# Kernel optimization log

Hardware: AMD Instinct MI355X
Metric: run time of the kernel (lower is better)

Reference implementation:

```python
import jax, jax.numpy as jnp
import numpy as np

B, N, C = 2, 2048, 1024
H = 16
DH = C // H
LN_EPS = 1e-5
NEG = -1e20


def setup_inputs() -> dict:
    key = jax.random.key(0)
    ks = jax.random.split(key, 8)
    s = 1.0 / np.sqrt(C)
    return {
        "query": jax.random.normal(ks[0], (B, N, C), dtype=jnp.float32),
        "key": jax.random.normal(ks[1], (B, N, C), dtype=jnp.float32),
        "value": jax.random.normal(ks[2], (B, N, C), dtype=jnp.float32),
        "attn_mask": jnp.ones((B, N), dtype=bool),
        # torch nn.Linear weights are [out, in]; y = x @ W.T
        "Wq": jax.random.uniform(ks[3], (C, C), jnp.float32, -s, s),
        "Wk": jax.random.uniform(ks[4], (C, C), jnp.float32, -s, s),
        "Wv": jax.random.uniform(ks[5], (C, C), jnp.float32, -s, s),
        "Wo": jax.random.uniform(ks[6], (C, C), jnp.float32, -s, s),
        "ln_g": jnp.ones((C,), jnp.float32),
        "ln_b": jnp.zeros((C,), jnp.float32),
    }


def reference(query, key, value, attn_mask, Wq, Wk, Wv, Wo, ln_g, ln_b):
    residual = query
    # projections + head split: [B,N,C] -> [B,H,N,DH]
    q = (query @ Wq.T).reshape(B, N, H, DH).transpose(0, 2, 1, 3)
    k = (key @ Wk.T).reshape(B, N, H, DH).transpose(0, 2, 1, 3)
    v = (value @ Wv.T).reshape(B, N, H, DH).transpose(0, 2, 1, 3)
    # NOTE: source computes scale but never applies it
    scores = jnp.einsum("bhqd,bhkd->bhqk", q, k)  # [B,H,N,N]
    # self-attention branch: outer-product mask [B,N,N]
    m2 = attn_mask[:, :, None] & attn_mask[:, None, :]
    scores = jnp.where(m2[:, None, :, :], scores, NEG)
    # NOTE: source uses nn.Softmax(dim=2) on 4D tensor -> softmax over QUERY axis
    attn = jax.nn.softmax(scores, axis=2)
    ctx = jnp.einsum("bhqk,bhkd->bhqd", attn, v)  # [B,H,N,DH]
    ctx = ctx.transpose(0, 2, 1, 3).reshape(B, N, C)
    out = ctx @ Wo.T
    x = residual + out
    mu = jnp.mean(x, axis=-1, keepdims=True)
    var = jnp.var(x, axis=-1, keepdims=True)
    return (x - mu) * jax.lax.rsqrt(var + LN_EPS) * ln_g + ln_b
```

## Files before the change

kernel.cpp:

```cpp
#include <hip/hip_runtime.h>
#include <hip/hip_bf16.h>

#define Bb 2
#define Nn 2048
#define Cc 1024
#define Hh 16
#define DHh 64

#define LOG2E 1.44269504088896340736f

typedef __attribute__((ext_vector_type(8))) short s16x8;
typedef __attribute__((ext_vector_type(4))) float f32x4;
typedef __attribute__((ext_vector_type(16))) float f32x16;

__device__ inline unsigned short f2bf(float f) {
  union { float f; unsigned u; } v; v.f = f;
  unsigned r = v.u + 0x7FFFu + ((v.u >> 16) & 1u);
  return (unsigned short)(r >> 16);
}
__device__ inline float bf2f(unsigned short h) {
  union { unsigned u; float f; } v; v.u = ((unsigned)h) << 16;
  return v.f;
}
__device__ inline float fast_exp2(float x) { return __builtin_amdgcn_exp2f(x); }

__device__ inline void gload16(const unsigned short* g, unsigned short* lds) {
  __builtin_amdgcn_global_load_lds(
      (const __attribute__((address_space(1))) unsigned int*)g,
      (__attribute__((address_space(3))) unsigned int*)lds, 16, 0, 0);
}

__device__ inline void barrier_lds_only() {
  asm volatile("s_waitcnt lgkmcnt(0)" ::: "memory");
  __builtin_amdgcn_s_barrier();
}

__device__ inline f32x4 mfma16(s16x8 a, s16x8 b, f32x4 c) {
  return __builtin_amdgcn_mfma_f32_16x16x32_bf16(a, b, c, 0, 0, 0);
}
__device__ inline f32x16 mfma32(s16x8 a, s16x8 b, f32x16 c) {
  return __builtin_amdgcn_mfma_f32_32x32x16_bf16(a, b, c, 0, 0, 0);
}

struct ConvArgs {
  const float* src[7];
  unsigned short* dst[7];
  int n[7];
  float scale[7];
};
__global__ __launch_bounds__(256) void conv_bf16(ConvArgs a) {
  const int y = blockIdx.y;
  const float* __restrict__ s = a.src[y];
  unsigned short* __restrict__ d = a.dst[y];
  const int n4 = a.n[y] >> 2;
  const float sc = a.scale[y];
  for (int i = blockIdx.x * 256 + threadIdx.x; i < n4; i += 1024 * 256) {
    f32x4 v = *(const f32x4*)(s + 4 * (size_t)i);
    ushort4 o;
    o.x = f2bf(v.x * sc); o.y = f2bf(v.y * sc);
    o.z = f2bf(v.z * sc); o.w = f2bf(v.w * sc);
    *(ushort4*)(d + 4 * (size_t)i) = o;
  }
}

__global__ __launch_bounds__(256) void gemm_qkv_bb(
    const unsigned short* __restrict__ Aq, const unsigned short* __restrict__ Ak,
    const unsigned short* __restrict__ Av,
    const unsigned short* __restrict__ Bq, const unsigned short* __restrict__ Bk,
    const unsigned short* __restrict__ Bv,
    unsigned short* __restrict__ Yq, unsigned short* __restrict__ Yk,
    unsigned short* __restrict__ Yv)
{
  __shared__ unsigned short As[3][128][32];
  __shared__ unsigned short Bs[3][128][32];

  const int bid = blockIdx.x + 8 * (blockIdx.y + 32 * blockIdx.z);
  const int swz = (bid & 7) * 96 + (bid >> 3);
  const int bx = swz & 7, by = (swz >> 3) & 31, bz = swz >> 8;

  const unsigned short* A = (bz == 0) ? Aq : (bz == 1) ? Ak : Av;
  const unsigned short* Bw = (bz == 0) ? Bq : (bz == 1) ? Bk : Bv;
  unsigned short* Y = (bz == 0) ? Yq : (bz == 1) ? Yk : Yv;

  const int tid = threadIdx.x;
  const int lane = tid & 63, wid = tid >> 6;
  const int r = lane & 15, g = lane >> 4;
  const int wr = wid >> 1, wc = wid & 1;
  const int m_blk = by * 128, n_blk = bx * 128;

  const int gr = wid * 16 + (lane >> 2);
  const int gc = (lane & 3) * 8;

  f32x4 acc[4][4] = {};

#pragma unroll
  for (int p = 0; p < 3; ++p) {
    gload16(A  + (size_t)(m_blk + gr)      * Cc + p * 32 + gc, &As[p][wid * 16][0]);
    gload16(A  + (size_t)(m_blk + 64 + gr) * Cc + p * 32 + gc, &As[p][64 + wid * 16][0]);
    gload16(Bw + (size_t)(n_blk + gr)      * Cc + p * 32 + gc, &Bs[p][wid * 16][0]);
    gload16(Bw + (size_t)(n_blk + 64 + gr) * Cc + p * 32 + gc, &Bs[p][64 + wid * 16][0]);
  }

  int cur = 0;
  for (int kt = 0; kt < 32; ++kt) {
    asm volatile("s_waitcnt vmcnt(8)" ::: "memory");
    __builtin_amdgcn_s_barrier();
    s16x8 av[4], bv[4];
#pragma unroll
    for (int i = 0; i < 4; ++i) av[i] = *(const s16x8*)&As[cur][wr * 64 + 16 * i + r][g * 8];
#pragma unroll
    for (int j = 0; j < 4; ++j) bv[j] = *(const s16x8*)&Bs[cur][wc * 64 + 16 * j + r][g * 8];
#pragma unroll
    for (int i = 0; i < 4; ++i)
#pragma unroll
      for (int j = 0; j < 4; ++j) acc[i][j] = mfma16(av[i], bv[j], acc[i][j]);
    asm volatile("s_barrier" ::: "memory");
    const int kn = (kt + 3 < 32) ? (kt + 3) * 32 : 0;
    gload16(A  + (size_t)(m_blk + gr)      * Cc + kn + gc, &As[cur][wid * 16][0]);
    gload16(A  + (size_t)(m_blk + 64 + gr) * Cc + kn + gc, &As[cur][64 + wid * 16][0]);
    gload16(Bw + (size_t)(n_blk + gr)      * Cc + kn + gc, &Bs[cur][wid * 16][0]);
    gload16(Bw + (size_t)(n_blk + 64 + gr) * Cc + kn + gc, &Bs[cur][64 + wid * 16][0]);
    cur = (cur == 2) ? 0 : cur + 1;
  }
#pragma unroll
  for (int i = 0; i < 4; ++i)
#pragma unroll
    for (int j = 0; j < 4; ++j)
#pragma unroll
      for (int t = 0; t < 4; ++t) {
        int row = m_blk + wr * 64 + 16 * i + 4 * g + t;
        int col = n_blk + wc * 64 + 16 * j + r;
        Y[(size_t)row * Cc + col] = f2bf(acc[i][j][t]);
      }
}

__global__ __launch_bounds__(256) void col_exp_fused(
    const unsigned short* __restrict__ Qb, const unsigned short* __restrict__ Kb,
    const unsigned short* __restrict__ Vb, unsigned short* __restrict__ Vtg)
{
  __shared__ unsigned short Qc[2][128][72];
  __shared__ float lsum[128];
  __shared__ float rl[128];
  const int tid = threadIdx.x;
  const int lane = tid & 63, w = tid >> 6;
  const int r = lane & 15, g = lane >> 4;
  const int k0 = blockIdx.x * 128;
  const int h = blockIdx.y, b = blockIdx.z;
  const size_t base = (size_t)b * Nn * Cc + (size_t)h * DHh;

  if (tid < 128) lsum[tid] = 0.f;
  s16x8 bv[2][8];
#pragma unroll
  for (int s = 0; s < 2; ++s)
#pragma unroll
    for (int j = 0; j < 8; ++j)
      bv[s][j] = *(const s16x8*)(Kb + base + (size_t)(k0 + 16 * j + r) * Cc + s * 32 + g * 8);

  const int srow = tid >> 3, sc8 = (tid & 7) * 8;
  s16x8 rQ[4];
#pragma unroll
  for (int it = 0; it < 4; ++it)
    rQ[it] = *(const s16x8*)(Qb + base + (size_t)(srow + 32 * it) * Cc + sc8);
#pragma unroll
  for (int it = 0; it < 4; ++it)
    *(s16x8*)&Qc[0][srow + 32 * it][sc8] = rQ[it];
#pragma unroll
  for (int it = 0; it < 4; ++it)
    rQ[it] = *(const s16x8*)(Qb + base + (size_t)(128 + srow + 32 * it) * Cc + sc8);
  __syncthreads();

  float esum[8] = {};
  for (int qc = 0; qc < Nn / 128; ++qc) {
    const int cur = qc & 1, nxt = cur ^ 1;
#pragma unroll
    for (int it = 0; it < 4; ++it)
      *(s16x8*)&Qc[nxt][srow + 32 * it][sc8] = rQ[it];
    s16x8 av[2][2];
#pragma unroll
    for (int s = 0; s < 2; ++s)
#pragma unroll
      for (int i = 0; i < 2; ++i)
        av[s][i] = *(const s16x8*)&Qc[cur][w * 32 + 16 * i + r][s * 32 + g * 8];
    const int qn = (qc + 2 < Nn / 128) ? (qc + 2) * 128 : 0;
#pragma unroll
    for (int it = 0; it < 4; ++it)
      rQ[it] = *(const s16x8*)(Qb + base + (size_t)(qn + srow + 32 * it) * Cc + sc8);
    f32x4 acc[2][8] = {};
    __builtin_amdgcn_s_setprio(1);
#pragma unroll
    for (int s = 0; s < 2; ++s)
#pragma unroll
      for (int i = 0; i < 2; ++i)
#pragma unroll
        for (int j = 0; j < 4; ++j) acc[i][j] = mfma16(av[s][i], bv[s][j], acc[i][j]);
    __builtin_amdgcn_s_setprio(0);
#pragma unroll
    for (int j = 0; j < 4; ++j)
#pragma unroll
      for (int i = 0; i < 2; ++i)
#pragma unroll
        for (int t = 0; t < 4; ++t) esum[j] += fast_exp2(acc[i][j][t]);
    __builtin_amdgcn_s_setprio(1);
#pragma unroll
    for (int s = 0; s < 2; ++s)
#pragma unroll
      for (int i = 0; i < 2; ++i)
#pragma unroll
        for (int j = 4; j < 8; ++j) acc[i][j] = mfma16(av[s][i], bv[s][j], acc[i][j]);
    __builtin_amdgcn_s_setprio(0);
#pragma unroll
    for (int j = 4; j < 8; ++j)
#pragma unroll
      for (int i = 0; i < 2; ++i)
#pragma unroll
        for (int t = 0; t < 4; ++t) esum[j] += fast_exp2(acc[i][j][t]);
    barrier_lds_only();
  }
#pragma unroll
  for (int j = 0; j < 8; ++j) {
    float e = esum[j];
    e += __shfl_xor(e, 16, 64);
    e += __shfl_xor(e, 32, 64);
    if (g == 0) atomicAdd(&lsum[16 * j + r], e);
  }
  __syncthreads();
  if (tid < 128) rl[tid] = 1.0f / lsum[tid];
  __syncthreads();
#pragma unroll
  for (int it = 0; it < 4; ++it) {
    int e = tid + 256 * it;
    int row = e >> 3, c8 = (e & 7) * 8;
    *(s16x8*)&Qc[0][row][c8] = *(const s16x8*)(Vb + base + (size_t)(k0 + row) * Cc + c8);
  }
  __syncthreads();
  const size_t vbase = (size_t)(b * Hh + h) * DHh * Nn;
#pragma unroll
  for (int it = 0; it < 4; ++it) {
    int f = tid + 256 * it;
    int d = f >> 4;
    int p8 = (f & 15) * 8;
    int sg = p8 >> 4;
    int hl = (p8 >> 3) & 1;
    s16x8 o;
#pragma unroll
    for (int u = 0; u < 8; ++u) {
      int k = 16 * sg + 4 * hl + (u & 3) + 8 * (u >> 2);
      o[u] = (short)f2bf(bf2f(Qc[0][k][d]) * rl[k]);
    }
    *(s16x8*)(Vtg + vbase + (size_t)d * Nn + k0 + p8) = o;
  }
}

__global__ __launch_bounds__(256, 4) void ctx_pv(
    const unsigned short* __restrict__ Qb, const unsigned short* __restrict__ Kb,
    const unsigned short* __restrict__ Vtg,
    unsigned short* __restrict__ Ctx0, unsigned short* __restrict__ Ctx1)
{
  __shared__ unsigned short Kt[2][64][72];
  __shared__ unsigned short Vt[2][64][72];
  const int tid = threadIdx.x;
  const int lane = tid & 63, w = tid >> 6;
  const int m = lane & 31;
  const int hl = lane >> 5;
  const int q0 = blockIdx.x * 128;
  const int h = blockIdx.y;
  const int b = blockIdx.z >> 1, half = blockIdx.z & 1;
  const int kstart = half * (Nn / 2);
  const size_t base = (size_t)b * Nn * Cc + (size_t)h * DHh;
  const size_t vbase = (size_t)(b * Hh + h) * DHh * Nn;

  s16x8 av[4];
#pragma unroll
  for (int s = 0; s < 4; ++s)
    av[s] = *(const s16x8*)(Qb + base + (size_t)(q0 + w * 32 + m) * Cc + s * 16 + hl * 8);

  const int srow = tid >> 3, sc8 = (tid & 7) * 8;
  s16x8 rK[2], rV[2];
#pragma unroll
  for (int it = 0; it < 2; ++it) {
    rK[it] = *(const s16x8*)(Kb + base + (size_t)(kstart + srow + 32 * it) * Cc + sc8);
    rV[it] = *(const s16x8*)(Vtg + vbase + (size_t)(srow + 32 * it) * Nn + kstart + sc8);
  }
#pragma unroll
  for (int it = 0; it < 2; ++it) {
    *(s16x8*)&Kt[0][srow + 32 * it][sc8] = rK[it];
    *(s16x8*)&Vt[0][srow + 32 * it][sc8] = rV[it];
  }
#pragma unroll
  for (int it = 0; it < 2; ++it) {
    rK[it] = *(const s16x8*)(Kb + base + (size_t)(kstart + 64 + srow + 32 * it) * Cc + sc8);
    rV[it] = *(const s16x8*)(Vtg + vbase + (size_t)(srow + 32 * it) * Nn + kstart + 64 + sc8);
  }
  __syncthreads();

  f32x16 acc2[2] = {};

  for (int kt = 0; kt < 16; ++kt) {
    const int cur = kt & 1, nxt = cur ^ 1;
#pragma unroll
    for (int it = 0; it < 2; ++it) {
      *(s16x8*)&Kt[nxt][srow + 32 * it][sc8] = rK[it];
      *(s16x8*)&Vt[nxt][srow + 32 * it][sc8] = rV[it];
    }
    const int kn = kstart + ((kt + 2 < 16) ? (kt + 2) * 64 : 0);
#pragma unroll
    for (int it = 0; it < 2; ++it) {
      rK[it] = *(const s16x8*)(Kb + base + (size_t)(kn + srow + 32 * it) * Cc + sc8);
      rV[it] = *(const s16x8*)(Vtg + vbase + (size_t)(srow + 32 * it) * Nn + kn + sc8);
    }
    f32x16 sa0 = {};
    __builtin_amdgcn_s_setprio(1);
#pragma unroll
    for (int s = 0; s < 4; ++s) {
      s16x8 kv = *(const s16x8*)&Kt[cur][m][s * 16 + hl * 8];
      sa0 = mfma32(kv, av[s], sa0);
    }
    __builtin_amdgcn_s_setprio(0);
    f32x16 sa1 = {};
    __builtin_amdgcn_s_setprio(1);
#pragma unroll
    for (int s = 0; s < 4; ++s) {
      s16x8 kv = *(const s16x8*)&Kt[cur][32 + m][s * 16 + hl * 8];
      sa1 = mfma32(kv, av[s], sa1);
    }
    __builtin_amdgcn_s_setprio(0);
    union { s16x8 v; unsigned int u[4]; } pf0[2];
#pragma unroll
    for (int g2 = 0; g2 < 2; ++g2)
#pragma unroll
      for (int p = 0; p < 4; ++p) {
        float e0 = fast_exp2(sa0[8 * g2 + 2 * p]);
        float e1 = fast_exp2(sa0[8 * g2 + 2 * p + 1]);
        pf0[g2].u[p] = __builtin_amdgcn_perm(__float_as_uint(e1), __float_as_uint(e0),
                                             0x07060302u);
      }
    __builtin_amdgcn_s_setprio(1);
#pragma unroll
    for (int g2 = 0; g2 < 2; ++g2)
#pragma unroll
      for (int j2 = 0; j2 < 2; ++j2) {
        s16x8 bv = *(const s16x8*)&Vt[cur][32 * j2 + m][g2 * 16 + hl * 8];
        acc2[j2] = mfma32(pf0[g2].v, bv, acc2[j2]);
      }
    __builtin_amdgcn_s_setprio(0);
    union { s16x8 v; unsigned int u[4]; } pf1[2];
#pragma unroll
    for (int g2 = 0; g2 < 2; ++g2)
#pragma unroll
      for (int p = 0; p < 4; ++p) {
        float e0 = fast_exp2(sa1[8 * g2 + 2 * p]);
        float e1 = fast_exp2(sa1[8 * g2 + 2 * p + 1]);
        pf1[g2].u[p] = __builtin_amdgcn_perm(__float_as_uint(e1), __float_as_uint(e0),
                                             0x07060302u);
      }
    __builtin_amdgcn_s_setprio(1);
#pragma unroll
    for (int g2 = 0; g2 < 2; ++g2)
#pragma unroll
      for (int j2 = 0; j2 < 2; ++j2) {
        s16x8 bv = *(const s16x8*)&Vt[cur][32 * j2 + m][(2 + g2) * 16 + hl * 8];
        acc2[j2] = mfma32(pf1[g2].v, bv, acc2[j2]);
      }
    __builtin_amdgcn_s_setprio(0);
    barrier_lds_only();
  }
  unsigned short* __restrict__ Cg = half ? Ctx1 : Ctx0;
#pragma unroll
  for (int j2 = 0; j2 < 2; ++j2)
#pragma unroll
    for (int t = 0; t < 16; ++t) {
      int qr = 32 * w + (t & 3) + 8 * (t >> 2) + 4 * hl;
      Cg[base + (size_t)(q0 + qr) * Cc + 32 * j2 + m] = f2bf(acc2[j2][t]);
    }
}

__global__ __launch_bounds__(512) void gemm_res_bb(
    const unsigned short* __restrict__ A0, const unsigned short* __restrict__ A1,
    const unsigned short* __restrict__ Bw,
    const float* __restrict__ resid, float* __restrict__ Yout)
{
  __shared__ unsigned short As[2][128][32];
  __shared__ unsigned short Bs[2][64][32];

  const int bid0 = blockIdx.x + 16 * blockIdx.y;
  const int swz = (bid0 & 7) * 64 + (bid0 >> 3);
  const int bx = swz & 15, by = swz >> 4;
  const int m_blk = by * 128, n_blk = bx * 64;

  const int tid = threadIdx.x;
  const int lane = tid & 63, wid = tid >> 6;
  const int r = lane & 15, g = lane >> 4;
  const int wr = wid >> 1, wc = wid & 1;

  const int arow = tid >> 2, ac8 = (tid & 3) * 8;
  const int grb = (wid & 3) * 16 + (lane >> 2), gcb = (lane & 3) * 8;

  f32x4 acc[2][2] = {};

  s16x8 rA0 = *(const s16x8*)(A0 + (size_t)(m_blk + arow) * Cc + ac8);
  s16x8 rA1 = *(const s16x8*)(A1 + (size_t)(m_blk + arow) * Cc + ac8);
  if (wid < 4)
    gload16(Bw + (size_t)(n_blk + grb) * Cc + gcb, &Bs[0][(wid & 3) * 16][0]);
  {
    s16x8 s0;
#pragma unroll
    for (int u = 0; u < 8; ++u)
      s0[u] = (short)f2bf(bf2f((unsigned short)rA0[u]) + bf2f((unsigned short)rA1[u]));
    *(s16x8*)&As[0][arow][ac8] = s0;
  }
  rA0 = *(const s16x8*)(A0 + (size_t)(m_blk + arow) * Cc + 32 + ac8);
  rA1 = *(const s16x8*)(A1 + (size_t)(m_blk + arow) * Cc + 32 + ac8);
  __syncthreads();

  int cur = 0;
  for (int k0 = 0; k0 < Cc; k0 += 32) {
    const int nxt = cur ^ 1;
    const int kn  = (k0 + 32 < Cc) ? k0 + 32 : 0;
    const int kn2 = (k0 + 64 < Cc) ? k0 + 64 : 0;
    if (wid < 4)
      gload16(Bw + (size_t)(n_blk + grb) * Cc + kn + gcb, &Bs[nxt][(wid & 3) * 16][0]);
    s16x8 nA0 = *(const s16x8*)(A0 + (size_t)(m_blk + arow) * Cc + kn2 + ac8);
    s16x8 nA1 = *(const s16x8*)(A1 + (size_t)(m_blk + arow) * Cc + kn2 + ac8);
    {
      s16x8 s0;
#pragma unroll
      for (int u = 0; u < 8; ++u)
        s0[u] = (short)f2bf(bf2f((unsigned short)rA0[u]) + bf2f((unsigned short)rA1[u]));
      *(s16x8*)&As[nxt][arow][ac8] = s0;
    }
    s16x8 av[2], bvv[2];
#pragma unroll
    for (int i = 0; i < 2; ++i) av[i] = *(const s16x8*)&As[cur][wr * 32 + 16 * i + r][g * 8];
#pragma unroll
    for (int j = 0; j < 2; ++j) bvv[j] = *(const s16x8*)&Bs[cur][wc * 32 + 16 * j + r][g * 8];
#pragma unroll
    for (int i = 0; i < 2; ++i)
#pragma unroll
      for (int j = 0; j < 2; ++j) acc[i][j] = mfma16(av[i], bvv[j], acc[i][j]);
    rA0 = nA0; rA1 = nA1;
    __syncthreads();
    cur = nxt;
  }
#pragma unroll
  for (int i = 0; i < 2; ++i)
#pragma unroll
    for (int j = 0; j < 2; ++j)
#pragma unroll
      for (int t = 0; t < 4; ++t) {
        size_t idx = (size_t)(m_blk + wr * 32 + 16 * i + 4 * g + t) * Cc
                   + (n_blk + wc * 32 + 16 * j + r);
        Yout[idx] = acc[i][j][t] + resid[idx];
      }
}

__global__ __launch_bounds__(256) void layernorm_inplace(
    float* __restrict__ X, const float* __restrict__ gam, const float* __restrict__ bet)
{
  const int row = blockIdx.x;
  const int tid = threadIdx.x;
  float* x = X + (size_t)row * Cc;
  f32x4 v = *(const f32x4*)(x + tid * 4);
  float s = v.x + v.y + v.z + v.w;
  float ss = v.x * v.x + v.y * v.y + v.z * v.z + v.w * v.w;
#pragma unroll
  for (int m = 1; m < 64; m <<= 1) { s += __shfl_xor(s, m, 64); ss += __shfl_xor(ss, m, 64); }
  __shared__ float red[8];
  const int w = tid >> 6, lane = tid & 63;
  if (lane == 0) { red[w] = s; red[4 + w] = ss; }
  __syncthreads();
  s  = red[0] + red[1] + red[2] + red[3];
  ss = red[4] + red[5] + red[6] + red[7];
  const float mean = s * (1.f / Cc);
  const float var  = ss * (1.f / Cc) - mean * mean;
  const float inv  = rsqrtf(var + 1e-5f);
  f32x4 gv = *(const f32x4*)(gam + tid * 4);
  f32x4 bv = *(const f32x4*)(bet + tid * 4);
  f32x4 o;
  o.x = (v.x - mean) * inv * gv.x + bv.x;
  o.y = (v.y - mean) * inv * gv.y + bv.y;
  o.z = (v.z - mean) * inv * gv.z + bv.z;
  o.w = (v.w - mean) * inv * gv.w + bv.w;
  *(f32x4*)(x + tid * 4) = o;
}

__global__ __launch_bounds__(256) void gemm_qkv_fb(
    const float* __restrict__ Xq, const float* __restrict__ Xk, const float* __restrict__ Xv,
    const float* __restrict__ Wq, const float* __restrict__ Wk, const float* __restrict__ Wv,
    unsigned short* __restrict__ Yq, unsigned short* __restrict__ Yk, unsigned short* __restrict__ Yv)
{
  __shared__ unsigned short As[128][40];
  __shared__ unsigned short Bs[128][40];
  const int z = blockIdx.z;
  const float* X = (z == 0) ? Xq : (z == 1) ? Xk : Xv;
  const float* W = (z == 0) ? Wq : (z == 1) ? Wk : Wv;
  unsigned short* Y = (z == 0) ? Yq : (z == 1) ? Yk : Yv;
  const float scale = (z == 0) ? LOG2E : 1.0f;

  const int tid = threadIdx.x;
  const int lane = tid & 63, wid = tid >> 6;
  const int r = lane & 15, g = lane >> 4;
  const int wr = wid >> 1, wc = wid & 1;
  const int m_blk = blockIdx.y * 128, n_blk = blockIdx.x * 128;

  f32x4 acc[4][4] = {};

  for (int k0 = 0; k0 < Cc; k0 += 32) {
    __syncthreads();
#pragma unroll
    for (int it = 0; it < 4; ++it) {
      int f = tid + 256 * it;
      int row = f >> 3, c4 = (f & 7) * 4;
      f32x4 xa = *(const f32x4*)(X + (size_t)(m_blk + row) * Cc + k0 + c4);
      ushort4 pa; pa.x = f2bf(xa.x); pa.y = f2bf(xa.y); pa.z = f2bf(xa.z); pa.w = f2bf(xa.w);
      *(ushort4*)&As[row][c4] = pa;
      f32x4 xb = *(const f32x4*)(W + (size_t)(n_blk + row) * Cc + k0 + c4);
      ushort4 pb; pb.x = f2bf(xb.x); pb.y = f2bf(xb.y); pb.z = f2bf(xb.z); pb.w = f2bf(xb.w);
      *(ushort4*)&Bs[row][c4] = pb;
    }
    __syncthreads();
    s16x8 av[4], bv[4];
#pragma unroll
    for (int i = 0; i < 4; ++i) av[i] = *(const s16x8*)&As[wr * 64 + 16 * i + r][g * 8];
#pragma unroll
    for (int j = 0; j < 4; ++j) bv[j] = *(const s16x8*)&Bs[wc * 64 + 16 * j + r][g * 8];
#pragma unroll
    for (int i = 0; i < 4; ++i)
#pragma unroll
      for (int j = 0; j < 4; ++j) acc[i][j] = mfma16(av[i], bv[j], acc[i][j]);
  }
#pragma unroll
  for (int i = 0; i < 4; ++i)
#pragma unroll
    for (int j = 0; j < 4; ++j)
#pragma unroll
      for (int t = 0; t < 4; ++t) {
        int row = m_blk + wr * 64 + 16 * i + 4 * g + t;
        int col = n_blk + wc * 64 + 16 * j + r;
        Y[(size_t)row * Cc + col] = f2bf(acc[i][j][t] * scale);
      }
}

__global__ __launch_bounds__(256) void ctx_pv_fb(
    const unsigned short* __restrict__ Qb, const unsigned short* __restrict__ Kb,
    const unsigned short* __restrict__ Vtg, unsigned short* __restrict__ Ctx)
{
  __shared__ unsigned short Kt[64][72];
  __shared__ unsigned short Vt[64][72];
  __shared__ unsigned short Qs[128][72];
  const int tid = threadIdx.x;
  const int lane = tid & 63, w = tid >> 6;
  const int m = lane & 31;
  const int hl = lane >> 5;
  const int q0 = blockIdx.x * 128;
  const int h = blockIdx.y, b = blockIdx.z;
  const size_t base = (size_t)b * Nn * Cc + (size_t)h * DHh;
  const size_t vbase = (size_t)(b * Hh + h) * DHh * Nn;

#pragma unroll
  for (int it = 0; it < 4; ++it) {
    int e = tid + 256 * it;
    int row = e >> 3, c8 = (e & 7) * 8;
    *(s16x8*)&Qs[row][c8] = *(const s16x8*)(Qb + base + (size_t)(q0 + row) * Cc + c8);
  }
  __syncthreads();
  s16x8 av[4];
#pragma unroll
  for (int s = 0; s < 4; ++s) av[s] = *(const s16x8*)&Qs[w * 32 + m][s * 16 + hl * 8];

  const int srow = tid >> 3, sc8 = (tid & 7) * 8;
  s16x8 rK[2], rV[2];
#pragma unroll
  for (int it = 0; it < 2; ++it) {
    rK[it] = *(const s16x8*)(Kb + base + (size_t)(srow + 32 * it) * Cc + sc8);
    rV[it] = *(const s16x8*)(Vtg + vbase + (size_t)(srow + 32 * it) * Nn + sc8);
  }

  f32x16 acc2[2] = {};

  for (int kt = 0; kt < Nn / 64; ++kt) {
    __syncthreads();
#pragma unroll
    for (int it = 0; it < 2; ++it) {
      *(s16x8*)&Kt[srow + 32 * it][sc8] = rK[it];
      *(s16x8*)&Vt[srow + 32 * it][sc8] = rV[it];
    }
    const int kn = (kt + 1 < Nn / 64) ? (kt + 1) * 64 : 0;
#pragma unroll
    for (int it = 0; it < 2; ++it) {
      rK[it] = *(const s16x8*)(Kb + base + (size_t)(kn + srow + 32 * it) * Cc + sc8);
      rV[it] = *(const s16x8*)(Vtg + vbase + (size_t)(srow + 32 * it) * Nn + kn + sc8);
    }
    __syncthreads();
#pragma unroll
    for (int kj = 0; kj < 2; ++kj) {
      f32x16 sa = {};
#pragma unroll
      for (int s = 0; s < 4; ++s) {
        s16x8 kv = *(const s16x8*)&Kt[32 * kj + m][s * 16 + hl * 8];
        sa = mfma32(kv, av[s], sa);
      }
#pragma unroll
      for (int g2 = 0; g2 < 2; ++g2) {
        union { s16x8 v; unsigned int u[4]; } pf;
#pragma unroll
        for (int p = 0; p < 4; ++p) {
          float e0 = fast_exp2(sa[8 * g2 + 2 * p]);
          float e1 = fast_exp2(sa[8 * g2 + 2 * p + 1]);
          pf.u[p] = __builtin_amdgcn_perm(__float_as_uint(e1), __float_as_uint(e0),
                                          0x07060302u);
        }
        const int sg = 2 * kj + g2;
#pragma unroll
        for (int j2 = 0; j2 < 2; ++j2) {
          s16x8 bv = *(const s16x8*)&Vt[32 * j2 + m][sg * 16 + hl * 8];
          acc2[j2] = mfma32(pf.v, bv, acc2[j2]);
        }
      }
    }
  }
#pragma unroll
  for (int j2 = 0; j2 < 2; ++j2)
#pragma unroll
    for (int t = 0; t < 16; ++t) {
      int qr = 32 * w + (t & 3) + 8 * (t >> 2) + 4 * hl;
      Ctx[base + (size_t)(q0 + qr) * Cc + 32 * j2 + m] = f2bf(acc2[j2][t]);
    }
}

__global__ __launch_bounds__(256) void gemm_res_fb(
    const unsigned short* __restrict__ Xb, const float* __restrict__ W,
    const float* __restrict__ resid, float* __restrict__ Yout)
{
  __shared__ unsigned short As[128][40];
  __shared__ unsigned short Bs[128][40];
  const int tid = threadIdx.x;
  const int lane = tid & 63, wid = tid >> 6;
  const int r = lane & 15, g = lane >> 4;
  const int wr = wid >> 1, wc = wid & 1;
  const int m_blk = blockIdx.y * 128, n_blk = blockIdx.x * 128;

  f32x4 acc[4][4] = {};

  for (int k0 = 0; k0 < Cc; k0 += 32) {
    __syncthreads();
#pragma unroll
    for (int it = 0; it < 2; ++it) {
      int f = tid + 256 * it;
      int row = f >> 2, c8 = (f & 3) * 8;
      *(s16x8*)&As[row][c8] = *(const s16x8*)(Xb + (size_t)(m_blk + row) * Cc + k0 + c8);
    }
#pragma unroll
    for (int it = 0; it < 4; ++it) {
      int f = tid + 256 * it;
      int row = f >> 3, c4 = (f & 7) * 4;
      f32x4 xb = *(const f32x4*)(W + (size_t)(n_blk + row) * Cc + k0 + c4);
      ushort4 pb; pb.x = f2bf(xb.x); pb.y = f2bf(xb.y); pb.z = f2bf(xb.z); pb.w = f2bf(xb.w);
      *(ushort4*)&Bs[row][c4] = pb;
    }
    __syncthreads();
    s16x8 av[4], bv[4];
#pragma unroll
    for (int i = 0; i < 4; ++i) av[i] = *(const s16x8*)&As[wr * 64 + 16 * i + r][g * 8];
#pragma unroll
    for (int j = 0; j < 4; ++j) bv[j] = *(const s16x8*)&Bs[wc * 64 + 16 * j + r][g * 8];
#pragma unroll
    for (int i = 0; i < 4; ++i)
#pragma unroll
      for (int j = 0; j < 4; ++j) acc[i][j] = mfma16(av[i], bv[j], acc[i][j]);
  }
#pragma unroll
  for (int i = 0; i < 4; ++i)
#pragma unroll
    for (int j = 0; j < 4; ++j)
#pragma unroll
      for (int t = 0; t < 4; ++t) {
        size_t idx = (size_t)(m_blk + wr * 64 + 16 * i + 4 * g + t) * Cc
                   + (n_blk + wc * 64 + 16 * j + r);
        Yout[idx] = acc[i][j][t] + resid[idx];
      }
}

extern "C" void kernel_launch(void* const* d_in, const int* in_sizes, int n_in,
                              void* d_out, int out_size, void* d_ws, size_t ws_size,
                              hipStream_t stream) {
  (void)in_sizes; (void)n_in; (void)out_size;
  const float* query = (const float*)d_in[0];
  const float* key_  = (const float*)d_in[1];
  const float* value = (const float*)d_in[2];
  const float* Wq = (const float*)d_in[4];
  const float* Wk = (const float*)d_in[5];
  const float* Wv = (const float*)d_in[6];
  const float* Wo = (const float*)d_in[7];
  const float* lg = (const float*)d_in[8];
  const float* lb = (const float*)d_in[9];
  float* out = (float*)d_out;

  char* ws = (char*)d_ws;
  unsigned short* Qb   = (unsigned short*)(ws);
  unsigned short* Kb   = (unsigned short*)(ws + (8u << 20));
  unsigned short* Vb   = (unsigned short*)(ws + (16u << 20));
  unsigned short* Vtg  = (unsigned short*)(ws + (24u << 20));

  const bool fast = ws_size >= (64ull << 20);
  if (fast) {
    unsigned short* Wqb  = (unsigned short*)(ws + (32ull << 20));
    unsigned short* Wkb  = (unsigned short*)(ws + (34ull << 20));
    unsigned short* Wvb  = (unsigned short*)(ws + (36ull << 20));
    unsigned short* Wob  = (unsigned short*)(ws + (38ull << 20));
    unsigned short* Xqb  = (unsigned short*)(ws + (40ull << 20));
    unsigned short* Xkb  = (unsigned short*)(ws + (48ull << 20));
    unsigned short* Xvb  = (unsigned short*)(ws + (56ull << 20));
    unsigned short* Ctx0 = (unsigned short*)(ws + (16ull << 20));
    unsigned short* Ctx1 = (unsigned short*)(ws + (40ull << 20));

    ConvArgs ca;
    ca.src[0] = query; ca.dst[0] = Xqb; ca.n[0] = Bb * Nn * Cc; ca.scale[0] = LOG2E;
    ca.src[1] = key_;  ca.dst[1] = Xkb; ca.n[1] = Bb * Nn * Cc; ca.scale[1] = 1.f;
    ca.src[2] = value; ca.dst[2] = Xvb; ca.n[2] = Bb * Nn * Cc; ca.scale[2] = 1.f;
    ca.src[3] = Wq;    ca.dst[3] = Wqb; ca.n[3] = Cc * Cc;      ca.scale[3] = 1.f;
    ca.src[4] = Wk;    ca.dst[4] = Wkb; ca.n[4] = Cc * Cc;      ca.scale[4] = 1.f;
    ca.src[5] = Wv;    ca.dst[5] = Wvb; ca.n[5] = Cc * Cc;      ca.scale[5] = 1.f;
    ca.src[6] = Wo;    ca.dst[6] = Wob; ca.n[6] = Cc * Cc;      ca.scale[6] = 1.f;
    conv_bf16<<<dim3(1024, 7), 256, 0, stream>>>(ca);

    gemm_qkv_bb<<<dim3(Cc / 128, (Bb * Nn) / 128, 3), 256, 0, stream>>>(
        Xqb, Xkb, Xvb, Wqb, Wkb, Wvb, Qb, Kb, Vb);
    col_exp_fused<<<dim3(Nn / 128, Hh, Bb), 256, 0, stream>>>(Qb, Kb, Vb, Vtg);
    ctx_pv<<<dim3(Nn / 128, Hh, Bb * 2), 256, 0, stream>>>(Qb, Kb, Vtg, Ctx0, Ctx1);
    gemm_res_bb<<<dim3(Cc / 64, (Bb * Nn) / 128), 512, 0, stream>>>(Ctx0, Ctx1, Wob, query, out);
    layernorm_inplace<<<Bb * Nn, 256, 0, stream>>>(out, lg, lb);
  } else {
    unsigned short* Ctx = (unsigned short*)(ws + (16u << 20));
    gemm_qkv_fb<<<dim3(Cc / 128, (Bb * Nn) / 128, 3), 256, 0, stream>>>(
        query, key_, value, Wq, Wk, Wv, Qb, Kb, Vb);
    col_exp_fused<<<dim3(Nn / 128, Hh, Bb), 256, 0, stream>>>(Qb, Kb, Vb, Vtg);
    ctx_pv_fb<<<dim3(Nn / 128, Hh, Bb), 256, 0, stream>>>(Qb, Kb, Vtg, Ctx);
    gemm_res_fb<<<dim3(Cc / 128, (Bb * Nn) / 128), 256, 0, stream>>>(Ctx, Wo, query, out);
    layernorm_inplace<<<Bb * Nn, 256, 0, stream>>>(out, lg, lb);
  }
}
```

Measured before the change: 265.7 us.

## Split ctx partial-sum add into separate kernel and triple-buffer output GEMM loads

The two partial context buffers are now summed by a standalone elementwise kernel into a new bf16 buffer, rather than being added inside the output projection GEMM's A-operand load path. The output GEMM then loads both A and W directly into LDS with async global-to-LDS loads through a three-stage ring buffer, synchronised with explicit vmcnt waits and barriers. Tiles shrink from 128x64 with 512 threads to 64x64 with 256 threads, doubling the block count. This removes per-iteration register conversions and adds latency hiding, at the cost of an extra launch and an extra 8 MB write plus read of the summed context.

```diff
diff --git a/kernel.cpp b/kernel.cpp
--- a/kernel.cpp
+++ b/kernel.cpp
@@ -374,72 +374,66 @@
     }
 }
 
-__global__ __launch_bounds__(512) void gemm_res_bb(
+__global__ __launch_bounds__(256) void ctx_add(
     const unsigned short* __restrict__ A0, const unsigned short* __restrict__ A1,
-    const unsigned short* __restrict__ Bw,
+    unsigned short* __restrict__ Y)
+{
+  const int i = blockIdx.x * 256 + threadIdx.x;
+  s16x8 a = *(const s16x8*)(A0 + 8 * (size_t)i);
+  s16x8 b = *(const s16x8*)(A1 + 8 * (size_t)i);
+  s16x8 o;
+#pragma unroll
+  for (int u = 0; u < 8; ++u)
+    o[u] = (short)f2bf(bf2f((unsigned short)a[u]) + bf2f((unsigned short)b[u]));
+  *(s16x8*)(Y + 8 * (size_t)i) = o;
+}
+
+__global__ __launch_bounds__(256) void gemm_res_bb(
+    const unsigned short* __restrict__ A, const unsigned short* __restrict__ Bw,
     const float* __restrict__ resid, float* __restrict__ Yout)
 {
-  __shared__ unsigned short As[2][128][32];
-  __shared__ unsigned short Bs[2][64][32];
-
-  const int bid0 = blockIdx.x + 16 * blockIdx.y;
-  const int swz = (bid0 & 7) * 64 + (bid0 >> 3);
+  __shared__ unsigned short As[3][64][32];
+  __shared__ unsigned short Bs[3][64][32];
+
+  const int bid = blockIdx.x + 16 * blockIdx.y;
+  const int swz = (bid & 7) * 128 + (bid >> 3);
   const int bx = swz & 15, by = swz >> 4;
-  const int m_blk = by * 128, n_blk = bx * 64;
+  const int m_blk = by * 64, n_blk = bx * 64;
 
   const int tid = threadIdx.x;
   const int lane = tid & 63, wid = tid >> 6;
   const int r = lane & 15, g = lane >> 4;
   const int wr = wid >> 1, wc = wid & 1;
 
-  const int arow = tid >> 2, ac8 = (tid & 3) * 8;
-  const int grb = (wid & 3) * 16 + (lane >> 2), gcb = (lane & 3) * 8;
+  const int gr = wid * 16 + (lane >> 2);
+  const int gc = (lane & 3) * 8;
 
   f32x4 acc[2][2] = {};
 
-  s16x8 rA0 = *(const s16x8*)(A0 + (size_t)(m_blk + arow) * Cc + ac8);
-  s16x8 rA1 = *(const s16x8*)(A1 + (size_t)(m_blk + arow) * Cc + ac8);
-  if (wid < 4)
-    gload16(Bw + (size_t)(n_blk + grb) * Cc + gcb, &Bs[0][(wid & 3) * 16][0]);
-  {
-    s16x8 s0;
-#pragma unroll
-    for (int u = 0; u < 8; ++u)
-      s0[u] = (short)f2bf(bf2f((unsigned short)rA0[u]) + bf2f((unsigned short)rA1[u]));
-    *(s16x8*)&As[0][arow][ac8] = s0;
-  }
-  rA0 = *(const s16x8*)(A0 + (size_t)(m_blk + arow) * Cc + 32 + ac8);
-  rA1 = *(const s16x8*)(A1 + (size_t)(m_blk + arow) * Cc + 32 + ac8);
-  __syncthreads();
+#pragma unroll
+  for (int p = 0; p < 3; ++p) {
+    gload16(A  + (size_t)(m_blk + gr) * Cc + p * 32 + gc, &As[p][wid * 16][0]);
+    gload16(Bw + (size_t)(n_blk + gr) * Cc + p * 32 + gc, &Bs[p][wid * 16][0]);
+  }
 
   int cur = 0;
-  for (int k0 = 0; k0 < Cc; k0 += 32) {
-    const int nxt = cur ^ 1;
-    const int kn  = (k0 + 32 < Cc) ? k0 + 32 : 0;
-    const int kn2 = (k0 + 64 < Cc) ? k0 + 64 : 0;
-    if (wid < 4)
-      gload16(Bw + (size_t)(n_blk + grb) * Cc + kn + gcb, &Bs[nxt][(wid & 3) * 16][0]);
-    s16x8 nA0 = *(const s16x8*)(A0 + (size_t)(m_blk + arow) * Cc + kn2 + ac8);
-    s16x8 nA1 = *(const s16x8*)(A1 + (size_t)(m_blk + arow) * Cc + kn2 + ac8);
-    {
-      s16x8 s0;
-#pragma unroll
-      for (int u = 0; u < 8; ++u)
-        s0[u] = (short)f2bf(bf2f((unsigned short)rA0[u]) + bf2f((unsigned short)rA1[u]));
-      *(s16x8*)&As[nxt][arow][ac8] = s0;
-    }
-    s16x8 av[2], bvv[2];
+  for (int kt = 0; kt < 32; ++kt) {
+    asm volatile("s_waitcnt vmcnt(4)" ::: "memory");
+    __builtin_amdgcn_s_barrier();
+    s16x8 av[2], bv[2];
 #pragma unroll
     for (int i = 0; i < 2; ++i) av[i] = *(const s16x8*)&As[cur][wr * 32 + 16 * i + r][g * 8];
 #pragma unroll
-    for (int j = 0; j < 2; ++j) bvv[j] = *(const s16x8*)&Bs[cur][wc * 32 + 16 * j + r][g * 8];
+    for (int j = 0; j < 2; ++j) bv[j] = *(const s16x8*)&Bs[cur][wc * 32 + 16 * j + r][g * 8];
 #pragma unroll
     for (int i = 0; i < 2; ++i)
 #pragma unroll
-      for (int j = 0; j < 2; ++j) acc[i][j] = mfma16(av[i], bvv[j], acc[i][j]);
-    rA0 = nA0; rA1 = nA1;
-    __syncthreads();
-    cur = nxt;
+      for (int j = 0; j < 2; ++j) acc[i][j] = mfma16(av[i], bv[j], acc[i][j]);
+    asm volatile("s_barrier" ::: "memory");
+    const int kn = (kt + 3 < 32) ? (kt + 3) * 32 : 0;
+    gload16(A  + (size_t)(m_blk + gr) * Cc + kn + gc, &As[cur][wid * 16][0]);
+    gload16(Bw + (size_t)(n_blk + gr) * Cc + kn + gc, &Bs[cur][wid * 16][0]);
+    cur = (cur == 2) ? 0 : cur + 1;
   }
 #pragma unroll
   for (int i = 0; i < 2; ++i)
@@ -712,6 +706,7 @@
     unsigned short* Xvb  = (unsigned short*)(ws + (56ull << 20));
     unsigned short* Ctx0 = (unsigned short*)(ws + (16ull << 20));
     unsigned short* Ctx1 = (unsigned short*)(ws + (40ull << 20));
+    unsigned short* CtxS = (unsigned short*)(ws + (48ull << 20));
 
     ConvArgs ca;
     ca.src[0] = query; ca.dst[0] = Xqb; ca.n[0] = Bb * Nn * Cc; ca.scale[0] = LOG2E;
@@ -727,7 +722,9 @@
         Xqb, Xkb, Xvb, Wqb, Wkb, Wvb, Qb, Kb, Vb);
     col_exp_fused<<<dim3(Nn / 128, Hh, Bb), 256, 0, stream>>>(Qb, Kb, Vb, Vtg);
     ctx_pv<<<dim3(Nn / 128, Hh, Bb * 2), 256, 0, stream>>>(Qb, Kb, Vtg, Ctx0, Ctx1);
-    gemm_res_bb<<<dim3(Cc / 64, (Bb * Nn) / 128), 512, 0, stream>>>(Ctx0, Ctx1, Wob, query, out);
+    ctx_add<<<(Bb * Nn * Cc) / (256 * 8), 256, 0, stream>>>(Ctx0, Ctx1, CtxS);
+    gemm_res_bb<<<dim3(Cc / 64, (Bb * Nn) / 64), 256, 0, stream>>>(
+        CtxS, Wob, query, out);
     layernorm_inplace<<<Bb * Nn, 256, 0, stream>>>(out, lg, lb);
   } else {
     unsigned short* Ctx = (unsigned short*)(ws + (16u << 20));
```

New measurement: 257.2 us. 3.2% less time.
